# Performance work log

Measured on AMD Instinct MI355X. Metric: run time of the kernel, lower is better.

Reference implementation:

```python
import jax, jax.numpy as jnp
import numpy as np

H, N, LMAX, KCH = 128, 64, 256, 2  # d_model, d_state, l_max per axis, kernel channels (bidirectional)


def _ssm_kernel(A_re, A_im, C_re, C_im, log_dt, L):
    """S4D diagonal SSM kernel (ZOH discretization) -> real kernel (KCH, H, L)."""
    A = A_re + 1j * A_im                      # (H, N)
    C = C_re + 1j * C_im                      # (KCH, H, N)
    dt = jnp.exp(log_dt)                      # (H,)
    dtA = dt[:, None] * A                     # (H, N)
    K = C * (jnp.exp(dtA) - 1.0) / A          # (KCH, H, N)
    vand = jnp.exp(dtA[:, :, None] * jnp.arange(L, dtype=dtA.real.dtype))  # (H, N, L)
    return 2.0 * jnp.einsum('chn,hnl->chl', K, vand).real


def _bidir_pad(k, L_in):
    """Split 2 kernel channels into fwd/bwd, flip backward one, pad to length Lk+L_in."""
    k0, k1 = k[:1], k[1:]                     # each (1, H, Lk)
    fwd = jnp.pad(k0, ((0, 0), (0, 0), (0, L_in)))
    bwd = jnp.pad(k1[..., ::-1], ((0, 0), (0, 0), (L_in, 0)))
    return fwd + bwd                          # (1, H, Lk + L_in)


def setup_inputs() -> dict:
    key = jax.random.key(0)
    ks = jax.random.split(key, 8)
    B, L1, L2 = 2, 256, 256
    u = jax.random.normal(ks[0], (B, H, L1, L2), jnp.float32)
    D = jax.random.normal(ks[1], (1, H), jnp.float32)

    def kparams(k_c, k_ci, k_dt):
        A_re = -0.5 * jnp.ones((H, N), jnp.float32)
        A_im = jnp.pi * jnp.broadcast_to(jnp.arange(N, dtype=jnp.float32), (H, N))
        C_re = jax.random.normal(k_c, (KCH, H, N), jnp.float32) * (0.5 ** 0.5)
        C_im = jax.random.normal(k_ci, (KCH, H, N), jnp.float32) * (0.5 ** 0.5)
        log_dt = jax.random.uniform(k_dt, (H,), jnp.float32,
                                    minval=np.log(1e-3), maxval=np.log(1e-1))
        return A_re, A_im, C_re, C_im, log_dt

    A_re0, A_im0, C_re0, C_im0, log_dt0 = kparams(ks[2], ks[3], ks[4])
    A_re1, A_im1, C_re1, C_im1, log_dt1 = kparams(ks[5], ks[6], ks[7])
    return {"u": u, "D": D,
            "A_re0": A_re0, "A_im0": A_im0, "C_re0": C_re0, "C_im0": C_im0, "log_dt0": log_dt0,
            "A_re1": A_re1, "A_im1": A_im1, "C_re1": C_re1, "C_im1": C_im1, "log_dt1": log_dt1}


def reference(u, D, A_re0, A_im0, C_re0, C_im0, log_dt0,
              A_re1, A_im1, C_re1, C_im1, log_dt1):
    B, _, L1, L2 = u.shape
    Lk1, Lk2 = min(L1, LMAX), min(L2, LMAX)
    # per-axis SSM kernels, then bidirectional flip-and-pad
    k1 = _bidir_pad(_ssm_kernel(A_re0, A_im0, C_re0, C_im0, log_dt0, Lk1), L1)  # (1,H,P1)
    k2 = _bidir_pad(_ssm_kernel(A_re1, A_im1, C_re1, C_im1, log_dt1, Lk2), L2)  # (1,H,P2)
    P1, P2 = L1 + Lk1, L2 + Lk2
    # N-D FFT convolution
    u_f = jnp.fft.rfftn(u, s=(P1, P2), axes=(-2, -1))        # (B,H,P1,P2//2+1)
    kf1 = jnp.fft.fft(k1, n=P1, axis=-1)                     # (1,H,P1) complex
    kf2 = jnp.fft.rfft(k2, n=P2, axis=-1)                    # (1,H,P2//2+1)
    k_f = jnp.einsum('chm,chn->chmn', kf1, kf2)              # outer product over axes (trank=1)
    y_f = jnp.einsum('bhmn,chmn->bchmn', u_f, k_f)           # (B,1,H,P1,P2r)
    y = jnp.fft.irfftn(y_f, s=(P1, P2), axes=(-2, -1))[..., :L1, :L2]
    # skip connection D
    y = y + jnp.einsum('bhxy,ch->bchxy', u, D)
    return y.reshape(B, -1, L1, L2)                          # (B, C*H, L1, L2)
```

## Files before the change

### kernel.cpp

```cpp
#include <hip/hip_runtime.h>

#define HH 128
#define NN 64
#define LL 256
#define WP 280

typedef __attribute__((ext_vector_type(8))) short bf8;
typedef __attribute__((ext_vector_type(4))) float f32x4;

__device__ inline ushort f2bf(float f) {
    uint x = __float_as_uint(f);
    return (ushort)((x + 0x7fffu + ((x >> 16) & 1u)) >> 16);
}
__device__ inline uint cvt_pk_bf16(float lo, float hi) {
    uint r;
    asm volatile("v_cvt_pk_bf16_f32 %0, %1, %2" : "=v"(r) : "v"(lo), "v"(hi));
    return r;
}
#define MFMA(a,b,c) __builtin_amdgcn_mfma_f32_16x16x32_bf16((a),(b),(c),0,0,0)

__global__ __launch_bounds__(512) void ssm_gen_fast(
    const float* __restrict__ A_re0, const float* __restrict__ A_im0,
    const float* __restrict__ C_re0, const float* __restrict__ C_im0,
    const float* __restrict__ log_dt0,
    const float* __restrict__ A_re1, const float* __restrict__ A_im1,
    const float* __restrict__ C_re1, const float* __restrict__ C_im1,
    const float* __restrict__ log_dt1,
    uint* __restrict__ arrg)
{
    __shared__ float4 par[128];
    __shared__ float  red[512];
    __shared__ ushort rev[512];

    int tid = threadIdx.x;
    int h   = blockIdx.x;
    int s   = blockIdx.y;

    if (tid < 128) {
        int n  = tid & 63;
        int ch = tid >> 6;
        const float* Ar = s ? A_re1 : A_re0;
        const float* Ai = s ? A_im1 : A_im0;
        const float* Cr = s ? C_re1 : C_re0;
        const float* Ci = s ? C_im1 : C_im0;
        const float* Ld = s ? log_dt1 : log_dt0;
        float dt = __expf(Ld[h]);
        float ar = Ar[h*NN + n], ai = Ai[h*NN + n];
        float cr = Cr[(ch*HH + h)*NN + n], ci = Ci[(ch*HH + h)*NN + n];
        float xr = dt * ar, xi = dt * ai;
        float phr = xi * 0.15915494f;
        float phf = phr - floorf(phr);
        float sn = __sinf(6.2831853f * phf);
        float cs = __cosf(6.2831853f * phf);
        float e  = __expf(xr);
        float er = e*cs - 1.f, ei = e*sn;
        float inv = 1.f / (ar*ar + ai*ai);
        float dr = (er*ar + ei*ai) * inv;
        float di = (ei*ar - er*ai) * inv;
        float Kr = 2.f*(cr*dr - ci*di);
        float Ki = 2.f*(cr*di + ci*dr);
        par[tid] = (float4){ xr, xi * 0.15915494f, Kr, Ki };
    }
    __syncthreads();

    {
        int l  = tid & 255;
        int ch = tid >> 8;
        float lf = (float)l;
#pragma unroll
        for (int nh = 0; nh < 2; ++nh) {
            const float4* pb = &par[ch*64 + nh*32];
            float acc = 0.f;
            for (int n = 0; n < 32; ++n) {
                float4 p = pb[n];
                float mag = __expf(p.x * lf);
                float ph  = p.y * lf;
                float phf = ph - floorf(ph);
                float ang = 6.2831853f * phf;
                acc += p.z * (mag * __cosf(ang)) - p.w * (mag * __sinf(ang));
            }
            if (nh == 0) red[tid] = acc;
            else {
                int ri = ch ? (256 + l) : (255 - l);
                rev[ri] = f2bf(red[tid] + acc);
            }
        }
    }
    __syncthreads();

    uint lo = rev[tid];
    uint hi = (tid < 511) ? (uint)rev[tid + 1] : 0u;
    arrg[(s*HH + h)*512 + tid] = lo | (hi << 16);
}

__global__ __launch_bounds__(512, 4) void s4nd_v3(
    const float* __restrict__ u, const float* __restrict__ Dv,
    const uint* __restrict__ arrg, float* __restrict__ out)
{
    __shared__ ushort WT[128 * WP];
    __shared__ uint   arr[2][512];

    int tid = threadIdx.x;

    int j    = blockIdx.x;
    int xcd  = j & 7;
    int k    = j >> 3;
    int bh   = xcd * 32 + (k >> 1);
    int y0   = (k & 1) * 128;
    int h    = bh & (HH - 1);

    arr[0][tid] = arrg[h*512 + tid];
    arr[1][tid] = arrg[(HH + h)*512 + tid];
    __syncthreads();

    int lane = tid & 63;
    int w = tid >> 6;
    int c = lane & 15, q = lane >> 4;

    f32x4 acc[16];
#pragma unroll
    for (int i = 0; i < 16; ++i) acc[i] = (f32x4){0.f,0.f,0.f,0.f};

    const float* ub = u + (size_t)bh * LL * LL;
    const float* rp0 = ub + (size_t)(w*32 +  0 + c) * LL;
    const float* rp1 = ub + (size_t)(w*32 + 16 + c) * LL;

    float4 A0, A1, A2, A3, B0, B1, B2, B3;
    {
        int yb = 8*q;
        A0 = *(const float4*)(rp0 + yb); A1 = *(const float4*)(rp0 + yb + 4);
        A2 = *(const float4*)(rp1 + yb); A3 = *(const float4*)(rp1 + yb + 4);
    }
#pragma unroll
    for (int kk = 0; kk < 8; ++kk) {
        if (kk < 7) {
            int ybn = (kk + 1)*32 + 8*q;
            B0 = *(const float4*)(rp0 + ybn); B1 = *(const float4*)(rp0 + ybn + 4);
            B2 = *(const float4*)(rp1 + ybn); B3 = *(const float4*)(rp1 + ybn + 4);
        }
        __builtin_amdgcn_sched_barrier(0);
        bf8 b0, b1;
        uint* p0 = (uint*)&b0; uint* p1 = (uint*)&b1;
        p0[0] = cvt_pk_bf16(A0.x, A0.y); p0[1] = cvt_pk_bf16(A0.z, A0.w);
        p0[2] = cvt_pk_bf16(A1.x, A1.y); p0[3] = cvt_pk_bf16(A1.z, A1.w);
        p1[0] = cvt_pk_bf16(A2.x, A2.y); p1[1] = cvt_pk_bf16(A2.z, A2.w);
        p1[2] = cvt_pk_bf16(A3.x, A3.y); p1[3] = cvt_pk_bf16(A3.z, A3.w);
        int sbase = 255 - y0 - c + kk*32 + 8*q;
        __builtin_amdgcn_s_setprio(1);
#pragma unroll
        for (int mi = 0; mi < 8; ++mi) {
            int s0 = sbase - 16*mi;
            bf8 a; uint* pa = (uint*)&a;
            pa[0] = arr[1][s0];     pa[1] = arr[1][s0 + 2];
            pa[2] = arr[1][s0 + 4]; pa[3] = arr[1][s0 + 6];
            acc[mi*2 + 0] = MFMA(a, b0, acc[mi*2 + 0]);
            acc[mi*2 + 1] = MFMA(a, b1, acc[mi*2 + 1]);
        }
        __builtin_amdgcn_s_setprio(0);
        A0 = B0; A1 = B1; A2 = B2; A3 = B3;
    }

#pragma unroll
    for (int mi = 0; mi < 8; ++mi)
#pragma unroll
        for (int ni = 0; ni < 2; ++ni)
#pragma unroll
            for (int r = 0; r < 4; ++r) {
                int row = 16*mi + 4*q + r;
                int col = w*32 + 16*ni + c;
                WT[row*WP + col] = f2bf(acc[mi*2 + ni][r]);
                acc[mi*2 + ni][r] = 0.f;
            }
    __syncthreads();

    int wm2 = (w >> 1) * 64, wn2 = (w & 1) * 64;
    float dh = Dv[h];
    float* yb_ = out + (size_t)bh * LL * LL;

#pragma unroll
    for (int half = 0; half < 2; ++half) {
        int nb = wn2 + half*32;

        float uh[32];
#pragma unroll
        for (int mi = 0; mi < 4; ++mi)
#pragma unroll
            for (int r = 0; r < 4; ++r) {
                int row = wm2 + 16*mi + 4*q + r;
#pragma unroll
                for (int ni = 0; ni < 2; ++ni)
                    uh[(mi*4 + r)*2 + ni] = ub[(size_t)row*LL + y0 + nb + 16*ni + c];
            }

#pragma unroll
        for (int kk = 0; kk < 8; ++kk) {
            int xb = kk*32;
            bf8 b0, b1;
            b0 = *(const bf8*)&WT[(nb + c)*WP + xb + 8*q];
            b1 = *(const bf8*)&WT[(nb + 16 + c)*WP + xb + 8*q];
            int sbase = 255 - wm2 - c + xb + 8*q;
            __builtin_amdgcn_s_setprio(1);
#pragma unroll
            for (int mi = 0; mi < 4; ++mi) {
                int s0 = sbase - 16*mi;
                bf8 a; uint* pa = (uint*)&a;
                pa[0] = arr[0][s0];     pa[1] = arr[0][s0 + 2];
                pa[2] = arr[0][s0 + 4]; pa[3] = arr[0][s0 + 6];
                acc[mi*2 + 0] = MFMA(a, b0, acc[mi*2 + 0]);
                acc[mi*2 + 1] = MFMA(a, b1, acc[mi*2 + 1]);
            }
            __builtin_amdgcn_s_setprio(0);
        }

#pragma unroll
        for (int mi = 0; mi < 4; ++mi)
#pragma unroll
            for (int ni = 0; ni < 2; ++ni)
#pragma unroll
                for (int r = 0; r < 4; ++r) {
                    int row = wm2 + 16*mi + 4*q + r;
                    int col = y0 + nb + 16*ni + c;
                    yb_[(size_t)row*LL + col] =
                        acc[mi*2 + ni][r] + dh * uh[(mi*4 + r)*2 + ni];
                    acc[mi*2 + ni][r] = 0.f;
                }
    }
}

extern "C" void kernel_launch(void* const* d_in, const int* in_sizes, int n_in,
                              void* d_out, int out_size, void* d_ws, size_t ws_size,
                              hipStream_t stream)
{
    const float* u       = (const float*)d_in[0];
    const float* D       = (const float*)d_in[1];
    const float* A_re0   = (const float*)d_in[2];
    const float* A_im0   = (const float*)d_in[3];
    const float* C_re0   = (const float*)d_in[4];
    const float* C_im0   = (const float*)d_in[5];
    const float* log_dt0 = (const float*)d_in[6];
    const float* A_re1   = (const float*)d_in[7];
    const float* A_im1   = (const float*)d_in[8];
    const float* C_re1   = (const float*)d_in[9];
    const float* C_im1   = (const float*)d_in[10];
    const float* log_dt1 = (const float*)d_in[11];
    float* out = (float*)d_out;

    uint* arrg = (uint*)d_ws;

    ssm_gen_fast<<<dim3(HH, 2), 512, 0, stream>>>(
        A_re0, A_im0, C_re0, C_im0, log_dt0,
        A_re1, A_im1, C_re1, C_im1, log_dt1, arrg);
    s4nd_v3<<<512, 512, 0, stream>>>(u, D, arrg, out);
}
```

Before: 44.23 us.

## Reuse Toeplitz A-fragments via register sliding window and widen second-stage tiles

The kernel-table layout is split into even/odd-parity halves, so each lane's Toeplitz A-operand becomes a contiguous window of uints. Those windows now sit in registers as a sliding buffer, and each step loads only two new fragments instead of re-reading LDS for every MFMA. The second-axis convolution processes all 64 columns in a single pass with 4 B-fragments reused across 4 A-fragments, and the skip-connection u values are read at store time instead of being prefetched. The u prefetch double-buffering in the first stage is removed, which may expose global load latency and raises register pressure under the 4-blocks occupancy bound.

```diff
diff --git a/kernel.cpp b/kernel.cpp
--- a/kernel.cpp
+++ b/kernel.cpp
@@ -88,12 +88,16 @@
     }
     __syncthreads();
 
-    uint lo = rev[tid];
-    uint hi = (tid < 511) ? (uint)rev[tid + 1] : 0u;
-    arrg[(s*HH + h)*512 + tid] = lo | (hi << 16);
-}
-
-__global__ __launch_bounds__(512, 4) void s4nd_v3(
+    {
+        int j  = tid & 255;
+        uint lo, hi;
+        if (tid < 256) { lo = rev[2*j];     hi = rev[2*j + 1]; }
+        else           { lo = rev[2*j + 1]; hi = (j == 255) ? 0u : (uint)rev[2*j + 2]; }
+        arrg[(s*HH + h)*512 + tid] = lo | (hi << 16);
+    }
+}
+
+__global__ __launch_bounds__(512, 4) void s4nd_v4(
     const float* __restrict__ u, const float* __restrict__ Dv,
     const uint* __restrict__ arrg, float* __restrict__ out)
 {
@@ -116,6 +120,12 @@
     int lane = tid & 63;
     int w = tid >> 6;
     int c = lane & 15, q = lane >> 4;
+    int wm2 = (w >> 1) * 64, wn2 = (w & 1) * 64;
+
+    const uint* T1 = &arr[0][(c & 1) ? 0 : 256];
+    const uint* T2 = &arr[1][(c & 1) ? 0 : 256];
+    int jb2 = (255 - y0  - c + 8*q) >> 1;
+    int jb1 = (255 - wm2 - c + 8*q) >> 1;
 
     f32x4 acc[16];
 #pragma unroll
@@ -125,39 +135,42 @@
     const float* rp0 = ub + (size_t)(w*32 +  0 + c) * LL;
     const float* rp1 = ub + (size_t)(w*32 + 16 + c) * LL;
 
-    float4 A0, A1, A2, A3, B0, B1, B2, B3;
-    {
-        int yb = 8*q;
-        A0 = *(const float4*)(rp0 + yb); A1 = *(const float4*)(rp0 + yb + 4);
-        A2 = *(const float4*)(rp1 + yb); A3 = *(const float4*)(rp1 + yb + 4);
+    bf8 win[8];
+#pragma unroll
+    for (int t = -7; t <= 0; ++t) {
+        int jj = jb2 + 8*t;
+        uint* pw = (uint*)&win[t & 7];
+        pw[0] = T2[jj]; pw[1] = T2[jj+1]; pw[2] = T2[jj+2]; pw[3] = T2[jj+3];
     }
 #pragma unroll
     for (int kk = 0; kk < 8; ++kk) {
-        if (kk < 7) {
-            int ybn = (kk + 1)*32 + 8*q;
-            B0 = *(const float4*)(rp0 + ybn); B1 = *(const float4*)(rp0 + ybn + 4);
-            B2 = *(const float4*)(rp1 + ybn); B3 = *(const float4*)(rp1 + ybn + 4);
-        }
-        __builtin_amdgcn_sched_barrier(0);
+        if (kk) {
+#pragma unroll
+            for (int t = 2*kk - 1; t <= 2*kk; ++t) {
+                int jj = jb2 + 8*t;
+                uint* pw = (uint*)&win[t & 7];
+                pw[0] = T2[jj]; pw[1] = T2[jj+1]; pw[2] = T2[jj+2]; pw[3] = T2[jj+3];
+            }
+        }
+        int yb = kk*32 + 8*q;
+        float4 A0 = *(const float4*)(rp0 + yb);
+        float4 A1 = *(const float4*)(rp0 + yb + 4);
+        float4 A2 = *(const float4*)(rp1 + yb);
+        float4 A3 = *(const float4*)(rp1 + yb + 4);
         bf8 b0, b1;
         uint* p0 = (uint*)&b0; uint* p1 = (uint*)&b1;
         p0[0] = cvt_pk_bf16(A0.x, A0.y); p0[1] = cvt_pk_bf16(A0.z, A0.w);
         p0[2] = cvt_pk_bf16(A1.x, A1.y); p0[3] = cvt_pk_bf16(A1.z, A1.w);
         p1[0] = cvt_pk_bf16(A2.x, A2.y); p1[1] = cvt_pk_bf16(A2.z, A2.w);
         p1[2] = cvt_pk_bf16(A3.x, A3.y); p1[3] = cvt_pk_bf16(A3.z, A3.w);
-        int sbase = 255 - y0 - c + kk*32 + 8*q;
         __builtin_amdgcn_s_setprio(1);
 #pragma unroll
         for (int mi = 0; mi < 8; ++mi) {
-            int s0 = sbase - 16*mi;
-            bf8 a; uint* pa = (uint*)&a;
-            pa[0] = arr[1][s0];     pa[1] = arr[1][s0 + 2];
-            pa[2] = arr[1][s0 + 4]; pa[3] = arr[1][s0 + 6];
+            bf8 a = win[(2*kk - mi) & 7];
             acc[mi*2 + 0] = MFMA(a, b0, acc[mi*2 + 0]);
             acc[mi*2 + 1] = MFMA(a, b1, acc[mi*2 + 1]);
         }
         __builtin_amdgcn_s_setprio(0);
-        A0 = B0; A1 = B1; A2 = B2; A3 = B3;
     }
 
 #pragma unroll
@@ -173,58 +186,52 @@
             }
     __syncthreads();
 
-    int wm2 = (w >> 1) * 64, wn2 = (w & 1) * 64;
+    bf8 win2[4];
+#pragma unroll
+    for (int t = -3; t <= 0; ++t) {
+        int jj = jb1 + 8*t;
+        uint* pw = (uint*)&win2[t & 3];
+        pw[0] = T1[jj]; pw[1] = T1[jj+1]; pw[2] = T1[jj+2]; pw[3] = T1[jj+3];
+    }
+#pragma unroll
+    for (int kk = 0; kk < 8; ++kk) {
+        if (kk) {
+#pragma unroll
+            for (int t = 2*kk - 1; t <= 2*kk; ++t) {
+                int jj = jb1 + 8*t;
+                uint* pw = (uint*)&win2[t & 3];
+                pw[0] = T1[jj]; pw[1] = T1[jj+1]; pw[2] = T1[jj+2]; pw[3] = T1[jj+3];
+            }
+        }
+        int xb = kk*32;
+        bf8 b[4];
+#pragma unroll
+        for (int ni = 0; ni < 4; ++ni)
+            b[ni] = *(const bf8*)&WT[(wn2 + 16*ni + c)*WP + xb + 8*q];
+        __builtin_amdgcn_s_setprio(1);
+#pragma unroll
+        for (int mi = 0; mi < 4; ++mi) {
+            bf8 a = win2[(2*kk - mi) & 3];
+#pragma unroll
+            for (int ni = 0; ni < 4; ++ni)
+                acc[mi*4 + ni] = MFMA(a, b[ni], acc[mi*4 + ni]);
+        }
+        __builtin_amdgcn_s_setprio(0);
+    }
+
     float dh = Dv[h];
     float* yb_ = out + (size_t)bh * LL * LL;
-
-#pragma unroll
-    for (int half = 0; half < 2; ++half) {
-        int nb = wn2 + half*32;
-
-        float uh[32];
-#pragma unroll
-        for (int mi = 0; mi < 4; ++mi)
+#pragma unroll
+    for (int mi = 0; mi < 4; ++mi)
+#pragma unroll
+        for (int ni = 0; ni < 4; ++ni)
 #pragma unroll
             for (int r = 0; r < 4; ++r) {
                 int row = wm2 + 16*mi + 4*q + r;
-#pragma unroll
-                for (int ni = 0; ni < 2; ++ni)
-                    uh[(mi*4 + r)*2 + ni] = ub[(size_t)row*LL + y0 + nb + 16*ni + c];
-            }
-
-#pragma unroll
-        for (int kk = 0; kk < 8; ++kk) {
-            int xb = kk*32;
-            bf8 b0, b1;
-            b0 = *(const bf8*)&WT[(nb + c)*WP + xb + 8*q];
-            b1 = *(const bf8*)&WT[(nb + 16 + c)*WP + xb + 8*q];
-            int sbase = 255 - wm2 - c + xb + 8*q;
-            __builtin_amdgcn_s_setprio(1);
-#pragma unroll
-            for (int mi = 0; mi < 4; ++mi) {
-                int s0 = sbase - 16*mi;
-                bf8 a; uint* pa = (uint*)&a;
-                pa[0] = arr[0][s0];     pa[1] = arr[0][s0 + 2];
-                pa[2] = arr[0][s0 + 4]; pa[3] = arr[0][s0 + 6];
-                acc[mi*2 + 0] = MFMA(a, b0, acc[mi*2 + 0]);
-                acc[mi*2 + 1] = MFMA(a, b1, acc[mi*2 + 1]);
-            }
-            __builtin_amdgcn_s_setprio(0);
-        }
-
-#pragma unroll
-        for (int mi = 0; mi < 4; ++mi)
-#pragma unroll
-            for (int ni = 0; ni < 2; ++ni)
-#pragma unroll
-                for (int r = 0; r < 4; ++r) {
-                    int row = wm2 + 16*mi + 4*q + r;
-                    int col = y0 + nb + 16*ni + c;
-                    yb_[(size_t)row*LL + col] =
-                        acc[mi*2 + ni][r] + dh * uh[(mi*4 + r)*2 + ni];
-                    acc[mi*2 + ni][r] = 0.f;
-                }
-    }
+                int col = y0 + wn2 + 16*ni + c;
+                size_t o = (size_t)row * LL + col;
+                yb_[o] = acc[mi*4 + ni][r] + dh * ub[o];
+            }
 }
 
 extern "C" void kernel_launch(void* const* d_in, const int* in_sizes, int n_in,
@@ -250,5 +257,5 @@
     ssm_gen_fast<<<dim3(HH, 2), 512, 0, stream>>>(
         A_re0, A_im0, C_re0, C_im0, log_dt0,
         A_re1, A_im1, C_re1, C_im1, log_dt1, arrg);
-    s4nd_v3<<<512, 512, 0, stream>>>(u, D, arrg, out);
-}
+    s4nd_v4<<<512, 512, 0, stream>>>(u, D, arrg, out);
+}
```

Result: slower. 49.45 us (+11.8%).
